# Optimization experiments

Measured on AMD Instinct MI355X. Metric: run time of the kernel, lower is better.

Reference implementation:

```python
import jax, jax.numpy as jnp
import numpy as np

D_MODEL = 1024
NUM_HEADS = 16
D_K = D_MODEL // NUM_HEADS


def setup_inputs() -> dict:
    key = jax.random.key(0)
    ks = jax.random.split(key, 16)
    B, S, D = 4, 2048, D_MODEL
    scale = 1.0 / np.sqrt(D)
    inp = {
        'Xs': jax.random.normal(ks[0], (B, S, D), jnp.float32),
        'Xt': jax.random.normal(ks[1], (B, S, D), jnp.float32),
    }
    names = ['qs', 'qt', 'ks', 'kt', 'vs', 'vt']
    for i, n in enumerate(names):
        inp['W_' + n] = jax.random.normal(ks[2 + 2 * i], (D, D), jnp.float32) * scale
        inp['b_' + n] = jax.random.normal(ks[3 + 2 * i], (D,), jnp.float32) * 0.01
    inp['attn_bias'] = jnp.zeros((1, 1, 1, 1), jnp.float32)
    return inp


def _split_heads(x):
    B, S, _ = x.shape
    return x.reshape(B, S, NUM_HEADS, D_K).transpose(0, 2, 1, 3)  # (B,H,S,dk)


def reference(Xs, Xt, W_qs, b_qs, W_qt, b_qt, W_ks, b_ks, W_kt, b_kt,
              W_vs, b_vs, W_vt, b_vt, attn_bias):
    # Dual-linear fused projections: Linear(x) = x @ W.T + b (torch convention)
    Q = Xs @ W_qs.T + b_qs + Xt @ W_qt.T + b_qt
    K = Xs @ W_ks.T + b_ks + Xt @ W_kt.T + b_kt
    V = Xs @ W_vs.T + b_vs + Xt @ W_vt.T + b_vt
    Q, K, V = _split_heads(Q), _split_heads(K), _split_heads(V)
    scores = jnp.einsum('bhqd,bhkd->bhqk', Q, K) / jnp.sqrt(jnp.float32(D_K))
    scores = scores + attn_bias  # scalar learned bias, broadcast
    probs = jax.nn.softmax(scores, axis=-1)
    out = jnp.einsum('bhqk,bhkd->bhqd', probs, V)  # (B,H,S,dk)
    B, H, S, dk = out.shape
    return out.transpose(0, 2, 1, 3).reshape(B, S, H * dk)
```

## Files before the change

### kernel.cpp

```cpp
#include <hip/hip_runtime.h>
#include <hip/hip_bf16.h>

typedef __bf16 bf16;
typedef __attribute__((ext_vector_type(8))) __bf16 bf16x8;
typedef __attribute__((ext_vector_type(4))) __bf16 bf16x4;
typedef __attribute__((ext_vector_type(4))) float f32x4;

#define D_MODEL 1024
#define NHEAD 16
#define DK 64
#define BB 4
#define SS 2048
#define MM 8192
#define KK 2048
#define NN 3072

#define LDP 72
#define QSCALE 0.18033688011112042f

__device__ __forceinline__ void glds16(const bf16* g, bf16* s) {
    __builtin_amdgcn_global_load_lds(
        (const __attribute__((address_space(1))) void*)g,
        (__attribute__((address_space(3))) void*)s, 16, 0, 0);
}

__device__ __forceinline__ void pack_chunk(const float* __restrict__ src,
                                           bf16* __restrict__ dst,
                                           int row_off, int col_off, int idx) {
    int m = idx >> 7;
    int cl = idx & 127;
    const float4* s4 = (const float4*)&src[((size_t)m << 10) + cl * 8];
    float4 v0 = s4[0], v1 = s4[1];
    bf16x8 o;
    o[0]=(bf16)v0.x; o[1]=(bf16)v0.y; o[2]=(bf16)v0.z; o[3]=(bf16)v0.w;
    o[4]=(bf16)v1.x; o[5]=(bf16)v1.y; o[6]=(bf16)v1.z; o[7]=(bf16)v1.w;
    int r = row_off + m;
    int k = col_off + cl * 8;
    int mi = r & 127, mt = r >> 7;
    int c = (k >> 3) & 7, kt = k >> 6;
    int slot = mi * 8 + (c ^ (mi & 7));
    *(bf16x8*)&dst[(((((size_t)mt * 32 + kt) << 10) + slot) << 3)] = o;
}

__global__ void pack_all(const float* __restrict__ Xs, const float* __restrict__ Xt,
                         const float* __restrict__ Wqs, const float* __restrict__ Wqt,
                         const float* __restrict__ Wks, const float* __restrict__ Wkt,
                         const float* __restrict__ Wvs, const float* __restrict__ Wvt,
                         const float* __restrict__ bqs, const float* __restrict__ bqt,
                         const float* __restrict__ bks, const float* __restrict__ bkt,
                         const float* __restrict__ bvs, const float* __restrict__ bvt,
                         bf16* __restrict__ Xp, bf16* __restrict__ Wp,
                         float* __restrict__ biasc) {
    int blk = blockIdx.x;
    if (blk < 8192) {
        int i = blk * 256 + threadIdx.x;
        int sel = i >> 20;
        int idx = i & 1048575;
        pack_chunk(sel ? Xt : Xs, Xp, 0, sel ? 1024 : 0, idx);
        return;
    }
    if (blk < 11264) {
        int i = (blk - 8192) * 256 + threadIdx.x;
        int gi = i >> 17;
        int idx = i & 131071;
        const float* src = (gi == 0) ? Wqs : (gi == 1) ? Wqt : (gi == 2) ? Wks
                         : (gi == 3) ? Wkt : (gi == 4) ? Wvs : Wvt;
        pack_chunk(src, Wp, (gi >> 1) * 1024, (gi & 1) * 1024, idx);
        return;
    }
    for (int n = threadIdx.x; n < NN; n += 256) {
        int g = n >> 10, c = n & 1023;
        const float* a = (g == 0) ? bqs : ((g == 1) ? bks : bvs);
        const float* b = (g == 0) ? bqt : ((g == 1) ? bkt : bvt);
        biasc[n] = a[c] + b[c];
    }
}

#define VM6 asm volatile("s_waitcnt vmcnt(6)" ::: "memory")
#define VM0 asm volatile("s_waitcnt vmcnt(0)" ::: "memory")
#define VMNONE
#define LGKM0 asm volatile("s_waitcnt lgkmcnt(0)" ::: "memory")

#define STG(gsrc, ldst) do {                                                  \
    glds16((gsrc) + ((size_t)t << 3), (ldst) + (w << 9));                     \
    glds16((gsrc) + (((size_t)t + 512) << 3), (ldst) + ((w + 8) << 9));       \
  } while (0)

#define TILE(P, KT, DO_STAGE, VMOP) do {                                      \
    const bf16* aP = &sA[P][wm << 6];                                         \
    const bf16* bP = &sB[P][bH][bR << 6];                                     \
    bf16x8 aF[4][2], bF[4][2];                                                \
    _Pragma("unroll")                                                         \
    for (int mi = 0; mi < 4; mi++)                                            \
      aF[mi][0] = *(const bf16x8*)&aP[((mi*16+l16)<<6) + ((quad^swz)<<3)];    \
    _Pragma("unroll")                                                         \
    for (int ni = 0; ni < 4; ni++)                                            \
      bF[ni][0] = *(const bf16x8*)&bP[((ni*16+l16)<<6) + ((quad^swz)<<3)];    \
    _Pragma("unroll")                                                         \
    for (int mi = 0; mi < 4; mi++)                                            \
      aF[mi][1] = *(const bf16x8*)&aP[((mi*16+l16)<<6) + (((4+quad)^swz)<<3)];\
    _Pragma("unroll")                                                         \
    for (int ni = 0; ni < 4; ni++)                                            \
      bF[ni][1] = *(const bf16x8*)&bP[((ni*16+l16)<<6) + (((4+quad)^swz)<<3)];\
    __builtin_amdgcn_s_setprio(1);                                            \
    _Pragma("unroll")                                                         \
    for (int mi = 0; mi < 4; mi++)                                            \
      _Pragma("unroll")                                                       \
      for (int ni = 0; ni < 4; ni++)                                          \
        acc[mi][ni] = __builtin_amdgcn_mfma_f32_16x16x32_bf16(                \
            aF[mi][0], bF[ni][0], acc[mi][ni], 0, 0, 0);                      \
    __builtin_amdgcn_s_setprio(0);                                            \
    LGKM0;                                                                    \
    __builtin_amdgcn_sched_barrier(0);                                        \
    __builtin_amdgcn_s_barrier();                                             \
    __builtin_amdgcn_sched_barrier(0);                                        \
    if (DO_STAGE) {                                                           \
      STG(Ag  + ((size_t)((KT) + 2) << 13), &sA[P][0]);                       \
      STG(Bg0 + ((size_t)((KT) + 2) << 13), &sB[P][0][0]);                    \
      STG(Bg1 + ((size_t)((KT) + 2) << 13), &sB[P][1][0]);                    \
    }                                                                         \
    __builtin_amdgcn_s_setprio(1);                                            \
    _Pragma("unroll")                                                         \
    for (int mi = 0; mi < 4; mi++)                                            \
      _Pragma("unroll")                                                       \
      for (int ni = 0; ni < 4; ni++)                                          \
        acc[mi][ni] = __builtin_amdgcn_mfma_f32_16x16x32_bf16(                \
            aF[mi][1], bF[ni][1], acc[mi][ni], 0, 0, 0);                      \
    __builtin_amdgcn_s_setprio(0);                                            \
    VMOP;                                                                     \
    __builtin_amdgcn_s_barrier();                                             \
    __builtin_amdgcn_sched_barrier(0);                                        \
  } while (0)

__global__ __launch_bounds__(512, 2) void gemm_qkv(
    const bf16* __restrict__ Xp, const bf16* __restrict__ Wp,
    const float* __restrict__ biasc,
    bf16* __restrict__ Qb, bf16* __restrict__ Kb, bf16* __restrict__ Vt) {
    __shared__ __align__(16) bf16 sA[2][8192];
    __shared__ __align__(16) bf16 sB[2][2][8192];

    const int t = threadIdx.x, lane = t & 63, w = t >> 6;
    const int quad = lane >> 4, l16 = lane & 15, swz = l16 & 7;
    const int wq = w & 3;
    const int wm = (w >> 2) * 64;
    const int wn = wq * 64;
    const int bH = wq >> 1;
    const int bR = (wq & 1) * 64;

    const int bx = blockIdx.x, by = blockIdx.y;
    const bf16* Ag  = Xp + (((size_t)bx * 32) << 13);
    const bf16* Bg0 = Wp + (((size_t)(by * 2 + 0) * 32) << 13);
    const bf16* Bg1 = Wp + (((size_t)(by * 2 + 1) * 32) << 13);

    f32x4 acc[4][4] = {};

    STG(Ag, &sA[0][0]); STG(Bg0, &sB[0][0][0]); STG(Bg1, &sB[0][1][0]);
    STG(Ag + 8192, &sA[1][0]); STG(Bg0 + 8192, &sB[1][0][0]); STG(Bg1 + 8192, &sB[1][1][0]);
    VM6;
    __builtin_amdgcn_s_barrier();
    __builtin_amdgcn_sched_barrier(0);

    int kt = 0;
#pragma unroll 1
    for (int i = 0; i < 15; i++, kt += 2) {
        TILE(0, kt, 1, VM6);
        TILE(1, kt + 1, 1, VM6);
    }
    TILE(0, 30, 0, VM0);
    TILE(1, 31, 0, VMNONE);

    const int g = by >> 2;
    const int m00 = bx << 7, n00 = by << 8;
#pragma unroll
    for (int mi = 0; mi < 4; mi++) {
        int mbase = m00 + wm + mi * 16 + quad * 4;
#pragma unroll
        for (int ni = 0; ni < 4; ni++) {
            int n = n00 + wn + ni * 16 + l16;
            float bias = biasc[n];
            int c = n & 1023, h = c >> 6, d = c & 63;
#pragma unroll
            for (int r = 0; r < 4; r++) {
                int m = mbase + r;
                int b = m >> 11, s = m & 2047;
                size_t bh = (size_t)(b * NHEAD + h);
                float v = acc[mi][ni][r] + bias;
                if (g == 0)
                    Qb[(bh * SS + s) * DK + d] = (bf16)(v * QSCALE);
                else if (g == 1)
                    Kb[(bh * SS + s) * DK + d] = (bf16)v;
                else
                    Vt[(bh * DK + d) * SS + s] = (bf16)v;
            }
        }
    }
}

__global__ __launch_bounds__(256) void attn(
    const bf16* __restrict__ Qb, const bf16* __restrict__ Kb,
    const bf16* __restrict__ Vt, float* __restrict__ out) {
    __shared__ __align__(16) bf16 sK[64 * 64];
    __shared__ __align__(16) bf16 sV[64 * 64];
    __shared__ __align__(16) bf16 sP[4][32 * LDP];

    const int lid = blockIdx.x + gridDim.x * blockIdx.y;
    const int bh = (lid & 7) * 8 + ((lid >> 3) & 7);
    const int q0 = (lid >> 6) * 128;

    const int t = threadIdx.x;
    const int lane = t & 63, w = t >> 6;
    const int quad = lane >> 4, l16 = lane & 15, swz = l16 & 7;
    const int b = bh >> 4, h = bh & 15;

    const bf16* Qp = Qb + ((size_t)bh * SS + q0 + w * 32) * DK;
    bf16x8 qf[2][2];
#pragma unroll
    for (int f = 0; f < 2; f++)
#pragma unroll
        for (int kb = 0; kb < 2; kb++)
            qf[f][kb] = *(const bf16x8*)&Qp[(f * 16 + l16) * DK + kb * 32 + quad * 8];

    f32x4 o[2][4] = {};
    float lsum[2] = {0.f, 0.f};

    const bf16* Kp = Kb + (size_t)bh * SS * DK;
    const bf16* Vp = Vt + (size_t)bh * DK * SS;

    for (int kt = 0; kt < SS; kt += 64) {
#pragma unroll
        for (int j = 0; j < 2; j++) {
            int u = (w * 2 + j) * 64 + lane;
            int row = u >> 3;
            int cc = (u & 7) ^ (row & 7);
            glds16(Kp + (size_t)(kt + row) * DK + cc * 8, &sK[(w * 2 + j) * 512]);
            glds16(Vp + (size_t)row * SS + kt + cc * 8, &sV[(w * 2 + j) * 512]);
        }
        __syncthreads();

        f32x4 st[2][4] = {};
#pragma unroll
        for (int kb = 0; kb < 2; kb++)
#pragma unroll
            for (int ki = 0; ki < 4; ki++) {
                bf16x8 kf = *(const bf16x8*)&sK[(ki * 16 + l16) * 64 + (((kb * 4 + quad) ^ swz) * 8)];
                st[0][ki] = __builtin_amdgcn_mfma_f32_16x16x32_bf16(kf, qf[0][kb], st[0][ki], 0, 0, 0);
                st[1][ki] = __builtin_amdgcn_mfma_f32_16x16x32_bf16(kf, qf[1][kb], st[1][ki], 0, 0, 0);
            }

#pragma unroll
        for (int f = 0; f < 2; f++) {
            float ls = 0.f;
#pragma unroll
            for (int ki = 0; ki < 4; ki++) {
                float p0 = __builtin_amdgcn_exp2f(st[f][ki][0]);
                float p1 = __builtin_amdgcn_exp2f(st[f][ki][1]);
                float p2 = __builtin_amdgcn_exp2f(st[f][ki][2]);
                float p3 = __builtin_amdgcn_exp2f(st[f][ki][3]);
                ls += (p0 + p1) + (p2 + p3);
                bf16x4 pk;
                pk[0] = (bf16)p0; pk[1] = (bf16)p1; pk[2] = (bf16)p2; pk[3] = (bf16)p3;
                *(bf16x4*)&sP[w][(f * 16 + l16) * LDP + ki * 16 + quad * 4] = pk;
            }
            lsum[f] += ls;
        }

#pragma unroll
        for (int kb = 0; kb < 2; kb++) {
            bf16x8 af0 = *(const bf16x8*)&sP[w][(l16) * LDP + kb * 32 + quad * 8];
            bf16x8 af1 = *(const bf16x8*)&sP[w][(16 + l16) * LDP + kb * 32 + quad * 8];
#pragma unroll
            for (int ni = 0; ni < 4; ni++) {
                bf16x8 vf = *(const bf16x8*)&sV[(ni * 16 + l16) * 64 + (((kb * 4 + quad) ^ swz) * 8)];
                o[0][ni] = __builtin_amdgcn_mfma_f32_16x16x32_bf16(af0, vf, o[0][ni], 0, 0, 0);
                o[1][ni] = __builtin_amdgcn_mfma_f32_16x16x32_bf16(af1, vf, o[1][ni], 0, 0, 0);
            }
        }
        __syncthreads();
    }

#pragma unroll
    for (int f = 0; f < 2; f++) {
        lsum[f] += __shfl_xor(lsum[f], 16);
        lsum[f] += __shfl_xor(lsum[f], 32);
    }

    float* op = out + ((size_t)(b * SS + q0 + w * 32)) * D_MODEL + h * DK;
#pragma unroll
    for (int f = 0; f < 2; f++)
#pragma unroll
        for (int r = 0; r < 4; r++) {
            float linv = 1.0f / __shfl(lsum[f], quad * 4 + r);
#pragma unroll
            for (int ni = 0; ni < 4; ni++)
                op[(f * 16 + quad * 4 + r) * D_MODEL + ni * 16 + l16] = o[f][ni][r] * linv;
        }
}

extern "C" void kernel_launch(void* const* d_in, const int* in_sizes, int n_in,
                              void* d_out, int out_size, void* d_ws, size_t ws_size,
                              hipStream_t stream) {
    const float* Xs   = (const float*)d_in[0];
    const float* Xt   = (const float*)d_in[1];
    const float* Wqs  = (const float*)d_in[2];
    const float* bqs  = (const float*)d_in[3];
    const float* Wqt  = (const float*)d_in[4];
    const float* bqt  = (const float*)d_in[5];
    const float* Wks  = (const float*)d_in[6];
    const float* bks  = (const float*)d_in[7];
    const float* Wkt  = (const float*)d_in[8];
    const float* bkt  = (const float*)d_in[9];
    const float* Wvs  = (const float*)d_in[10];
    const float* bvs  = (const float*)d_in[11];
    const float* Wvt  = (const float*)d_in[12];
    const float* bvt  = (const float*)d_in[13];
    float* out = (float*)d_out;

    char* ws = (char*)d_ws;
    bf16*  Xp    = (bf16*)(ws);
    bf16*  Wp    = (bf16*)(ws + 33554432);
    float* biasc = (float*)(ws + 46137344);
    bf16*  Qb    = (bf16*)(ws + 46149632);
    bf16*  Kb    = (bf16*)(ws + 62926848);
    bf16*  Vt    = (bf16*)(ws + 79704064);

    pack_all<<<11265, 256, 0, stream>>>(Xs, Xt, Wqs, Wqt, Wks, Wkt, Wvs, Wvt,
                                        bqs, bqt, bks, bkt, bvs, bvt,
                                        Xp, Wp, biasc);

    gemm_qkv<<<dim3(MM / 128, NN / 256), 512, 0, stream>>>(Xp, Wp, biasc, Qb, Kb, Vt);

    attn<<<dim3(SS / 128, BB * NHEAD), 256, 0, stream>>>(Qb, Kb, Vt, out);
}
```

Measured before the change: 370.5 us.

## Double-buffer MFMA operand fragments in registers to overlap LDS reads with math

Restructures the GEMM main loop so each tile's LDS fragment reads for the next k-step are issued before the MFMAs of the current step. The A/B fragments alternate between two register sets. Each tile now has a single barrier instead of two. The aim is to hide LDS read latency behind matrix math. In exchange, the global-to-LDS prefetch wait tightens from vmcnt(6) to vmcnt(0) each tile, and twice as many fragment registers are live, which raises VGPR pressure under the 2-block launch bound.

```diff
diff --git a/kernel.cpp b/kernel.cpp
--- a/kernel.cpp
+++ b/kernel.cpp
@@ -86,47 +86,45 @@
     glds16((gsrc) + (((size_t)t + 512) << 3), (ldst) + ((w + 8) << 9));       \
   } while (0)
 
-#define TILE(P, KT, DO_STAGE, VMOP) do {                                      \
-    const bf16* aP = &sA[P][wm << 6];                                         \
-    const bf16* bP = &sB[P][bH][bR << 6];                                     \
-    bf16x8 aF[4][2], bF[4][2];                                                \
+#define RD16(Q, AO, BO) do {                                                  \
+    const bf16* aP = &sA[Q][wm << 6];                                         \
+    const bf16* bP = &sB[Q][bH][bR << 6];                                     \
     _Pragma("unroll")                                                         \
-    for (int mi = 0; mi < 4; mi++)                                            \
-      aF[mi][0] = *(const bf16x8*)&aP[((mi*16+l16)<<6) + ((quad^swz)<<3)];    \
+    for (int mi = 0; mi < 4; mi++) {                                          \
+      AO[mi][0] = *(const bf16x8*)&aP[((mi*16+l16)<<6) + ((quad^swz)<<3)];    \
+      AO[mi][1] = *(const bf16x8*)&aP[((mi*16+l16)<<6) + (((4+quad)^swz)<<3)];\
+    }                                                                         \
     _Pragma("unroll")                                                         \
-    for (int ni = 0; ni < 4; ni++)                                            \
-      bF[ni][0] = *(const bf16x8*)&bP[((ni*16+l16)<<6) + ((quad^swz)<<3)];    \
-    _Pragma("unroll")                                                         \
-    for (int mi = 0; mi < 4; mi++)                                            \
-      aF[mi][1] = *(const bf16x8*)&aP[((mi*16+l16)<<6) + (((4+quad)^swz)<<3)];\
-    _Pragma("unroll")                                                         \
-    for (int ni = 0; ni < 4; ni++)                                            \
-      bF[ni][1] = *(const bf16x8*)&bP[((ni*16+l16)<<6) + (((4+quad)^swz)<<3)];\
+    for (int ni = 0; ni < 4; ni++) {                                          \
+      BO[ni][0] = *(const bf16x8*)&bP[((ni*16+l16)<<6) + ((quad^swz)<<3)];    \
+      BO[ni][1] = *(const bf16x8*)&bP[((ni*16+l16)<<6) + (((4+quad)^swz)<<3)];\
+    }                                                                         \
+  } while (0)
+
+#define MM32(AI, BI) do {                                                     \
     __builtin_amdgcn_s_setprio(1);                                            \
     _Pragma("unroll")                                                         \
-    for (int mi = 0; mi < 4; mi++)                                            \
+    for (int kb = 0; kb < 2; kb++)                                            \
       _Pragma("unroll")                                                       \
-      for (int ni = 0; ni < 4; ni++)                                          \
-        acc[mi][ni] = __builtin_amdgcn_mfma_f32_16x16x32_bf16(                \
-            aF[mi][0], bF[ni][0], acc[mi][ni], 0, 0, 0);                      \
+      for (int mi = 0; mi < 4; mi++)                                          \
+        _Pragma("unroll")                                                     \
+        for (int ni = 0; ni < 4; ni++)                                        \
+          acc[mi][ni] = __builtin_amdgcn_mfma_f32_16x16x32_bf16(              \
+              AI[mi][kb], BI[ni][kb], acc[mi][ni], 0, 0, 0);                  \
     __builtin_amdgcn_s_setprio(0);                                            \
-    LGKM0;                                                                    \
-    __builtin_amdgcn_sched_barrier(0);                                        \
-    __builtin_amdgcn_s_barrier();                                             \
-    __builtin_amdgcn_sched_barrier(0);                                        \
+  } while (0)
+
+#define TILE(P, KT, AI, BI, AO, BO, DO_STAGE, VMOP) do {                      \
     if (DO_STAGE) {                                                           \
       STG(Ag  + ((size_t)((KT) + 2) << 13), &sA[P][0]);                       \
       STG(Bg0 + ((size_t)((KT) + 2) << 13), &sB[P][0][0]);                    \
       STG(Bg1 + ((size_t)((KT) + 2) << 13), &sB[P][1][0]);                    \
     }                                                                         \
-    __builtin_amdgcn_s_setprio(1);                                            \
-    _Pragma("unroll")                                                         \
-    for (int mi = 0; mi < 4; mi++)                                            \
-      _Pragma("unroll")                                                       \
-      for (int ni = 0; ni < 4; ni++)                                          \
-        acc[mi][ni] = __builtin_amdgcn_mfma_f32_16x16x32_bf16(                \
-            aF[mi][1], bF[ni][1], acc[mi][ni], 0, 0, 0);                      \
-    __builtin_amdgcn_s_setprio(0);                                            \
+    RD16(P ^ 1, AO, BO);                                                      \
+    __builtin_amdgcn_sched_barrier(0);                                        \
+    MM32(AI, BI);                                                             \
+    __builtin_amdgcn_sched_barrier(0);                                        \
+    LGKM0;                                                                    \
     VMOP;                                                                     \
     __builtin_amdgcn_s_barrier();                                             \
     __builtin_amdgcn_sched_barrier(0);                                        \
@@ -153,21 +151,27 @@
     const bf16* Bg1 = Wp + (((size_t)(by * 2 + 1) * 32) << 13);
 
     f32x4 acc[4][4] = {};
+    bf16x8 aX[4][2], bX[4][2], aY[4][2], bY[4][2];
 
     STG(Ag, &sA[0][0]); STG(Bg0, &sB[0][0][0]); STG(Bg1, &sB[0][1][0]);
     STG(Ag + 8192, &sA[1][0]); STG(Bg0 + 8192, &sB[1][0][0]); STG(Bg1 + 8192, &sB[1][1][0]);
     VM6;
     __builtin_amdgcn_s_barrier();
     __builtin_amdgcn_sched_barrier(0);
+    RD16(0, aX, bX);
+    LGKM0;
+    VM0;
+    __builtin_amdgcn_s_barrier();
+    __builtin_amdgcn_sched_barrier(0);
 
     int kt = 0;
 #pragma unroll 1
     for (int i = 0; i < 15; i++, kt += 2) {
-        TILE(0, kt, 1, VM6);
-        TILE(1, kt + 1, 1, VM6);
-    }
-    TILE(0, 30, 0, VM0);
-    TILE(1, 31, 0, VMNONE);
+        TILE(0, kt,     aX, bX, aY, bY, 1, VM0);
+        TILE(1, kt + 1, aY, bY, aX, bX, 1, VM0);
+    }
+    TILE(0, 30, aX, bX, aY, bY, 0, VMNONE);
+    MM32(aY, bY);
 
     const int g = by >> 2;
     const int m00 = bx << 7, n00 = by << 8;
```

After: 366.0 us. No clear change (-1.2%).
